# Kernel optimization log

Hardware: AMD Instinct MI355X
Metric: run time of the kernel (lower is better)

## Reference

```python
import jax, jax.numpy as jnp
import numpy as np

D_MODEL = 1024
D_INNER = 2 * D_MODEL
D_STATE = 16
DT_RANK = (D_MODEL + 15) // 16  # math.ceil(d_model/16) = 64
D_CONV = 4
SEQ_L = 2048
BATCH = 2


def setup_inputs() -> dict:
    key = jax.random.key(0)
    ks = jax.random.split(key, 8)
    def w(k, shape, scale=0.02):
        return jax.random.normal(k, shape, dtype=jnp.float32) * scale
    x = jax.random.normal(ks[0], (SEQ_L, BATCH, D_MODEL), dtype=jnp.float32)
    # weights stored as (in, out); torch Linear is x @ W.T with W (out, in)
    W_in = w(ks[1], (D_MODEL, 2 * D_INNER))
    W_conv = w(ks[2], (D_INNER, 1, D_CONV), 0.3)  # depthwise conv kernel (O, I/groups=1, K)
    b_conv = jnp.zeros((D_INNER,), jnp.float32)
    W_x = w(ks[3], (D_INNER, DT_RANK + 2 * D_STATE))
    W_dt = w(ks[4], (DT_RANK, D_INNER))
    b_dt = jnp.zeros((D_INNER,), jnp.float32)
    A_log = jnp.log(jnp.broadcast_to(jnp.arange(1, D_STATE + 1, dtype=jnp.float32),
                                     (D_INNER, D_STATE)))
    D = jnp.ones((D_INNER,), jnp.float32)
    W_out = w(ks[5], (D_INNER, D_MODEL))
    return {"x": x, "W_in": W_in, "W_conv": W_conv, "b_conv": b_conv,
            "W_x": W_x, "W_dt": W_dt, "b_dt": b_dt,
            "A_log": A_log, "D": D, "W_out": W_out}


def _mamba_forward(x, W_in, W_conv, b_conv, W_x, W_dt, b_dt, A_log, D, W_out):
    xb = jnp.transpose(x, (1, 0, 2))                       # (b, l, d_model)
    b, l, _ = xb.shape
    x_and_res = xb @ W_in                                  # (b, l, 2*d_inner)
    xs, res = jnp.split(x_and_res, 2, axis=-1)
    # depthwise causal conv1d: torch pads d_conv-1 both sides then truncates to l
    xc = jnp.transpose(xs, (0, 2, 1))                      # (b, d_inner, l)
    xc = jax.lax.conv_general_dilated(
        xc, W_conv, window_strides=(1,), padding=[(D_CONV - 1, 0)],
        feature_group_count=D_INNER,
        dimension_numbers=("NCH", "OIH", "NCH")) + b_conv[None, :, None]
    u = jax.nn.silu(jnp.transpose(xc, (0, 2, 1)))          # (b, l, d_inner)
    # SSM parameters
    A = -jnp.exp(A_log)                                    # (d_inner, n)
    x_dbl = u @ W_x                                        # (b, l, dt_rank + 2n)
    delta, Bm, Cm = jnp.split(x_dbl, [DT_RANK, DT_RANK + D_STATE], axis=-1)
    delta = jax.nn.softplus(delta @ W_dt + b_dt)           # (b, l, d_inner)
    # selective scan: state (b, d_inner, n)
    def step(state, inp):
        d_t, B_t, C_t, u_t = inp                           # (b,d_in),(b,n),(b,n),(b,d_in)
        dA = jnp.exp(d_t[:, :, None] * A)                  # (b, d_inner, n)
        dBu = d_t[:, :, None] * B_t[:, None, :] * u_t[:, :, None]
        state = dA * state + dBu
        y_t = jnp.einsum("bdn,bn->bd", state, C_t)
        return state, y_t

    init = jnp.zeros((b, D_INNER, D_STATE), jnp.float32)
    seq = (jnp.moveaxis(delta, 1, 0), jnp.moveaxis(Bm, 1, 0),
           jnp.moveaxis(Cm, 1, 0), jnp.moveaxis(u, 1, 0))
    _, ys = jax.lax.scan(step, init, seq)                  # (l, b, d_inner)
    y = jnp.moveaxis(ys, 0, 1) + u * D                     # (b, l, d_inner)
    y = y * jax.nn.silu(res)
    return y @ W_out                                       # (b, l, d_model)


def reference(x, W_in, W_conv, b_conv, W_x, W_dt, b_dt, A_log, D, W_out):
    return _mamba_forward(x, W_in, W_conv, b_conv, W_x, W_dt, b_dt, A_log, D, W_out)
```

## Files before the change

kernel.cpp:

```cpp
#include <hip/hip_runtime.h>
#include <hip/hip_bf16.h>

#define L_SEQ  2048
#define NBATCH 2
#define DMODEL 1024
#define DINNER 2048
#define DSTATE 16
#define DTRANK 64
#define MROWS  (L_SEQ * NBATCH)
#define NCHUNK 64
#define LCHUNK 32
#define LOG2E  1.44269504f

using bf16 = __hip_bfloat16;
typedef short s16x8 __attribute__((ext_vector_type(8)));
typedef float f32x4 __attribute__((ext_vector_type(4)));

__device__ __forceinline__ void gload_lds16(const bf16* g, bf16* l) {
    __builtin_amdgcn_global_load_lds(
        (const __attribute__((address_space(1))) void*)g,
        (__attribute__((address_space(3))) void*)l, 16, 0, 0);
}

__device__ __forceinline__ float bf2f(short v) {
    return __uint_as_float(((unsigned)(unsigned short)v) << 16);
}

__global__ __launch_bounds__(512, 2)
void gemm256(const bf16* __restrict__ A, const bf16* __restrict__ Bt,
             bf16* __restrict__ C, int N, int K, int lda, int ldb)
{
    __shared__ __align__(16) bf16 As[2][256 * 64];
    __shared__ __align__(16) bf16 Bs[2][256 * 64];

    const int tid  = threadIdx.x;
    const int wid  = tid >> 6;
    const int lane = tid & 63;
    const int wr = wid >> 2, wc = wid & 3;
    const int fr = lane & 15, fk = lane >> 4;

    const int nbx = gridDim.x;
    const int nwg = nbx * gridDim.y;
    int id = blockIdx.y * nbx + blockIdx.x;
    int cpx = nwg >> 3;
    id = (id & 7) * cpx + (id >> 3);
    const long bm = (long)(id / nbx) * 256;
    const long bn = (long)(id % nbx) * 256;

    const int q0 = tid, q1 = tid + 512;
    const int r0 = q0 >> 3, r1 = q1 >> 3;
    const int c0 = ((q0 & 7) ^ (r0 & 7)) << 3;
    const int c1 = ((q1 & 7) ^ (r1 & 7)) << 3;
    const bf16* sA0h0 = A  + (bm + r0)       * (long)lda + c0;
    const bf16* sA1h0 = A  + (bm + r1)       * (long)lda + c1;
    const bf16* sA0h1 = A  + (bm + 128 + r0) * (long)lda + c0;
    const bf16* sA1h1 = A  + (bm + 128 + r1) * (long)lda + c1;
    const bf16* sB0h0 = Bt + (bn + r0)       * (long)ldb + c0;
    const bf16* sB1h0 = Bt + (bn + r1)       * (long)ldb + c1;
    const bf16* sB0h1 = Bt + (bn + 128 + r0) * (long)ldb + c0;
    const bf16* sB1h1 = Bt + (bn + 128 + r1) * (long)ldb + c1;
    const int dst0 = wid * 512;
    const int dst1 = 4096 + wid * 512;

    const int o0   = ((fk ^ (fr & 7)) << 3);
    const int o1   = o0 ^ 32;
    const int rA64 = (wr * 64 + fr) * 64;
    const int rB64 = (wc * 32 + fr) * 64;

    f32x4 acc[8][4] = {};
    s16x8 af[4][2], bf0[2][2], bf1[2][2];
    const int nt = K >> 6;

#define STAGE(ARR, BUF, H, P0, P1) do {                    \
        gload_lds16(P0, &ARR[BUF][(H) * 8192 + dst0]);     \
        gload_lds16(P1, &ARR[BUF][(H) * 8192 + dst1]);     \
        P0 += 64; P1 += 64;                                \
    } while (0)

#define LOADA(MH, CUR) do {                                   \
        const bf16* ab = &As[CUR][rA64 + (MH) * 8192];        \
        _Pragma("unroll") for (int m = 0; m < 4; ++m) {       \
            af[m][0] = *(const s16x8*)&ab[m * 1024 + o0];     \
            af[m][1] = *(const s16x8*)&ab[m * 1024 + o1]; }   \
    } while (0)

#define LOADB(NH, CUR, BF) do {                               \
        const bf16* bb = &Bs[CUR][rB64 + (NH) * 8192];        \
        _Pragma("unroll") for (int n = 0; n < 2; ++n) {       \
            BF[n][0] = *(const s16x8*)&bb[n * 1024 + o0];     \
            BF[n][1] = *(const s16x8*)&bb[n * 1024 + o1]; }   \
    } while (0)

#define MFMAQ(MH, NH, BF) do {                                               \
        __builtin_amdgcn_s_setprio(1);                                       \
        _Pragma("unroll") for (int ks = 0; ks < 2; ++ks)                     \
        _Pragma("unroll") for (int m = 0; m < 4; ++m)                        \
        _Pragma("unroll") for (int n = 0; n < 2; ++n)                        \
            acc[(MH) * 4 + m][(NH) * 2 + n] =                                \
                __builtin_amdgcn_mfma_f32_16x16x32_bf16(                     \
                    af[m][ks], BF[n][ks], acc[(MH) * 4 + m][(NH) * 2 + n],   \
                    0, 0, 0);                                                \
        __builtin_amdgcn_s_setprio(0);                                       \
    } while (0)

#define WB(NV) asm volatile("s_waitcnt vmcnt(" #NV ")\n\ts_barrier" ::: "memory")

    STAGE(As, 0, 0, sA0h0, sA1h0);
    STAGE(Bs, 0, 0, sB0h0, sB1h0);
    STAGE(Bs, 0, 1, sB0h1, sB1h1);
    STAGE(As, 0, 1, sA0h1, sA1h1);
    WB(4);

    int cur = 0;
    for (int t = 0; t < nt - 1; ++t) {
        STAGE(As, cur ^ 1, 0, sA0h0, sA1h0);
        LOADA(0, cur); LOADB(0, cur, bf0);
        MFMAQ(0, 0, bf0);  WB(4);
        STAGE(Bs, cur ^ 1, 0, sB0h0, sB1h0);
        LOADB(1, cur, bf1);
        MFMAQ(0, 1, bf1);  WB(4);
        STAGE(Bs, cur ^ 1, 1, sB0h1, sB1h1);
        LOADA(1, cur);
        MFMAQ(1, 1, bf1);
        STAGE(As, cur ^ 1, 1, sA0h1, sA1h1);
        MFMAQ(1, 0, bf0);  WB(4);
        cur ^= 1;
    }
    LOADA(0, cur); LOADB(0, cur, bf0);
    MFMAQ(0, 0, bf0);  WB(2);
    LOADB(1, cur, bf1);
    MFMAQ(0, 1, bf1);  WB(0);
    LOADA(1, cur);
    MFMAQ(1, 1, bf1);
    MFMAQ(1, 0, bf0);

#undef STAGE
#undef LOADA
#undef LOADB
#undef MFMAQ
#undef WB

    #pragma unroll
    for (int mh = 0; mh < 2; ++mh)
    #pragma unroll
    for (int m = 0; m < 4; ++m)
    #pragma unroll
    for (int nh = 0; nh < 2; ++nh)
    #pragma unroll
    for (int n = 0; n < 2; ++n) {
        f32x4 v = acc[mh * 4 + m][nh * 2 + n];
        long row0 = bm + wr * 64 + mh * 128 + m * 16 + fk * 4;
        long col  = bn + wc * 32 + nh * 128 + n * 16 + fr;
        #pragma unroll
        for (int j = 0; j < 4; ++j)
            C[(row0 + j) * N + col] = __float2bfloat16(v[j]);
    }
}

template<typename OutT, int EPI, bool SPLITK = false>
__global__ __launch_bounds__(256)
void gemm_bt(const bf16* __restrict__ A, const bf16* __restrict__ Bt,
             OutT* __restrict__ C, const float* __restrict__ bias,
             int M, int N, int K, int lda, int ldb)
{
    __shared__ __align__(16) bf16 As[2][128 * 32];
    __shared__ __align__(16) bf16 Bs[2][128 * 32];

    const int tid  = threadIdx.x;
    const int wave = tid >> 6;
    const int lane = tid & 63;
    const int wr = wave >> 1, wc = wave & 1;
    const int fr = lane & 15, fk = lane >> 4;

    const int nbx = gridDim.x;
    const int nwg = nbx * gridDim.y;
    int id  = blockIdx.y * nbx + blockIdx.x;
    if (nwg >= 8) {
        int cpx = nwg >> 3;
        id = (id & 7) * cpx + (id >> 3);
    }
    const int bxi = id % nbx, byi = id / nbx;
    const long bm = (long)byi * 128;
    const long bn = (long)bxi * 128;

    if constexpr (SPLITK) {
        long ko = (long)blockIdx.z * K;
        A  += ko;
        Bt += ko;
        C  += (size_t)blockIdx.z * M * N;
    }

    const int r0 = tid >> 2,         c0 = (tid & 3) << 3;
    const int r1 = (256 + tid) >> 2, c1 = c0;
    const bf16* pA0 = A  + (bm + r0) * (long)lda + c0;
    const bf16* pA1 = A  + (bm + r1) * (long)lda + c1;
    const bf16* pB0 = Bt + (bn + r0) * (long)ldb + c0;
    const bf16* pB1 = Bt + (bn + r1) * (long)ldb + c1;
    const size_t ld0 = (size_t)(wave * 64) * 8;
    const size_t ld1 = (size_t)(256 + wave * 64) * 8;

    f32x4 acc[4][4] = {};
    const int nt = K >> 5;

    gload_lds16(pA0, &As[0][ld0]);
    gload_lds16(pB0, &Bs[0][ld0]);
    gload_lds16(pA1, &As[0][ld1]);
    gload_lds16(pB1, &Bs[0][ld1]);
    pA0 += 32; pA1 += 32; pB0 += 32; pB1 += 32;
    __syncthreads();

    int cur = 0;
    for (int t = 0; t < nt; ++t) {
        if (t + 1 < nt) {
            gload_lds16(pA0, &As[cur ^ 1][ld0]);
            gload_lds16(pB0, &Bs[cur ^ 1][ld0]);
            gload_lds16(pA1, &As[cur ^ 1][ld1]);
            gload_lds16(pB1, &Bs[cur ^ 1][ld1]);
            pA0 += 32; pA1 += 32; pB0 += 32; pB1 += 32;
        }

        s16x8 afrag[4], bfrag[4];
        #pragma unroll
        for (int m = 0; m < 4; ++m)
            afrag[m] = *(const s16x8*)&As[cur][(wr * 64 + m * 16 + fr) * 32 + fk * 8];
        #pragma unroll
        for (int n = 0; n < 4; ++n)
            bfrag[n] = *(const s16x8*)&Bs[cur][(wc * 64 + n * 16 + fr) * 32 + fk * 8];

        #pragma unroll
        for (int m = 0; m < 4; ++m)
            #pragma unroll
            for (int n = 0; n < 4; ++n)
                acc[m][n] = __builtin_amdgcn_mfma_f32_16x16x32_bf16(
                    afrag[m], bfrag[n], acc[m][n], 0, 0, 0);

        __syncthreads();
        cur ^= 1;
    }

    #pragma unroll
    for (int m = 0; m < 4; ++m)
        #pragma unroll
        for (int n = 0; n < 4; ++n) {
            f32x4 v = acc[m][n];
            long row0 = bm + wr * 64 + m * 16 + fk * 4;
            long col  = bn + wc * 64 + n * 16 + fr;
            #pragma unroll
            for (int j = 0; j < 4; ++j) {
                float val = v[j];
                if (EPI == 1) {
                    val += bias[col];
                    val = (val > 20.f) ? val : log1pf(__expf(val));
                }
                if constexpr (sizeof(OutT) == 2)
                    C[(row0 + j) * N + col] = __float2bfloat16(val);
                else
                    C[(row0 + j) * N + col] = val;
            }
        }
}

__global__ void transpose_bf16(const float* __restrict__ in, bf16* __restrict__ out,
                               int R, int C, int Cpad)
{
    __shared__ float tile[32][33];
    int cb = blockIdx.x * 32, rb = blockIdx.y * 32;
    int tx = threadIdx.x, ty = threadIdx.y;
    #pragma unroll
    for (int i = 0; i < 4; ++i) {
        int r = rb + ty + i * 8, c = cb + tx;
        tile[ty + i * 8][tx] = (r < R && c < C) ? in[(long)r * C + c] : 0.f;
    }
    __syncthreads();
    #pragma unroll
    for (int i = 0; i < 4; ++i) {
        int oc = cb + ty + i * 8;
        int orow = rb + tx;
        if (oc < Cpad && orow < R)
            out[(long)oc * R + orow] = __float2bfloat16(tile[tx][ty + i * 8]);
    }
}

__global__ void convert_x_kernel(const float* __restrict__ x, bf16* __restrict__ Xb)
{
    int idx = blockIdx.x * 256 + threadIdx.x;
    int c   = idx & (DMODEL - 1);
    int row = idx >> 10;
    int l   = row & (L_SEQ - 1);
    int b   = row >> 11;
    Xb[idx] = __float2bfloat16(x[((l * NBATCH + b) << 10) | c]);
}

__global__ void conv_silu_kernel(const bf16* __restrict__ xr, const float* __restrict__ Wc,
                                 const float* __restrict__ bc, bf16* __restrict__ u)
{
    int idx = blockIdx.x * 256 + threadIdx.x;
    int g   = idx & 255;
    int row = idx >> 8;
    int c   = g << 3;
    int l   = row & (L_SEQ - 1);

    float acc[8];
    f32x4 bi0 = *(const f32x4*)(bc + c);
    f32x4 bi1 = *(const f32x4*)(bc + c + 4);
    #pragma unroll
    for (int j = 0; j < 4; ++j) { acc[j] = bi0[j]; acc[4 + j] = bi1[j]; }

    f32x4 w[8];
    #pragma unroll
    for (int j = 0; j < 8; ++j) w[j] = *(const f32x4*)(Wc + (c + j) * 4);

    #pragma unroll
    for (int t = 0; t < 4; ++t) {
        int ll = l - 3 + t;
        if (ll >= 0) {
            s16x8 v = *(const s16x8*)(xr + (long)(row - 3 + t) * 4096 + c);
            #pragma unroll
            for (int j = 0; j < 8; ++j)
                acc[j] += bf2f(v[j]) * w[j][t];
        }
    }
    s16x8 o;
    #pragma unroll
    for (int j = 0; j < 8; ++j) {
        float a = acc[j];
        float s = a / (1.f + __builtin_amdgcn_exp2f(-LOG2E * a));
        bf16 h = __float2bfloat16(s);
        o[j] = *(short*)&h;
    }
    *(s16x8*)(u + (long)row * DINNER + c) = o;
}

__global__ void reduce_xdbl(const float* __restrict__ part, float* __restrict__ xdbl,
                            bf16* __restrict__ drbf)
{
    int idx = blockIdx.x * 256 + threadIdx.x;
    const size_t stride = (size_t)MROWS * 128;
    float v = part[idx] + part[idx + stride] + part[idx + 2 * stride]
            + part[idx + 3 * stride];
    xdbl[idx] = v;
    int col = idx & 127;
    if (col < 64)
        drbf[(idx >> 7) * 64 + col] = __float2bfloat16(v);
}

__global__ void reduce_out(const float* __restrict__ part, float* __restrict__ out)
{
    int i = blockIdx.x * 256 + threadIdx.x;
    f32x4 a = ((const f32x4*)part)[i];
    f32x4 b = ((const f32x4*)(part + (size_t)MROWS * DMODEL))[i];
    ((f32x4*)out)[i] = a + b;
}

__global__ __launch_bounds__(256)
void scan_phase1(const float* __restrict__ delta, const bf16* __restrict__ u,
                 const float* __restrict__ xdbl, const float* __restrict__ A_log,
                 float* __restrict__ AS)
{
    const int idx   = blockIdx.x * 256 + threadIdx.x;
    const int half  = idx & 1;
    const int ch    = idx >> 1;
    const int chunk = blockIdx.y;
    const int d     = ch & (DINNER - 1);
    const int b     = ch >> 11;
    const int n0    = half * 8;

    float A2[8], s[8];
    const f32x4* Arow = (const f32x4*)(A_log + d * DSTATE + n0);
    #pragma unroll
    for (int q = 0; q < 2; ++q) {
        f32x4 v = Arow[q];
        #pragma unroll
        for (int j = 0; j < 4; ++j) A2[q * 4 + j] = -__expf(v[j]) * LOG2E;
    }
    #pragma unroll
    for (int n = 0; n < 8; ++n) s[n] = 0.f;
    float sdl = 0.f;

    bool fastA = true;
    #pragma unroll
    for (int j = 0; j < 8; ++j)
        fastA &= fabsf(A2[j] + (float)(n0 + j + 1) * LOG2E)
                 < 0.01f * (float)(n0 + j + 1);

    const long row0 = (long)b * L_SEQ + chunk * LCHUNK;
    const float* pD = delta + row0 * DINNER + d;
    const bf16*  pU = u     + row0 * DINNER + d;
    const f32x4* pB = (const f32x4*)(xdbl + row0 * 128 + 64 + n0);

    if (fastA) {
        #pragma unroll 4
        for (int l = 0; l < LCHUNK; ++l) {
            float dl = *pD;
            float uv = __bfloat162float(*pU);
            f32x4 B0 = pB[0], B1 = pB[1];
            pD += DINNER; pU += DINNER; pB += 32;
            float dbu = dl * uv;
            sdl += dl;
            float b1 = __builtin_amdgcn_exp2f(-LOG2E * dl);
            float b2 = b1 * b1, b3 = b2 * b1, b4 = b2 * b2;
            float b5 = b4 * b1, b6 = b4 * b2, b7 = b4 * b3, b8 = b4 * b4;
            float pre = half ? b8 : 1.f;
            s[0] = pre * b1 * s[0] + dbu * B0[0];
            s[1] = pre * b2 * s[1] + dbu * B0[1];
            s[2] = pre * b3 * s[2] + dbu * B0[2];
            s[3] = pre * b4 * s[3] + dbu * B0[3];
            s[4] = pre * b5 * s[4] + dbu * B1[0];
            s[5] = pre * b6 * s[5] + dbu * B1[1];
            s[6] = pre * b7 * s[6] + dbu * B1[2];
            s[7] = pre * b8 * s[7] + dbu * B1[3];
        }
    } else {
        #pragma unroll 4
        for (int l = 0; l < LCHUNK; ++l) {
            float dl = *pD;
            float uv = __bfloat162float(*pU);
            f32x4 B0 = pB[0], B1 = pB[1];
            pD += DINNER; pU += DINNER; pB += 32;
            float dbu = dl * uv;
            sdl += dl;
            #pragma unroll
            for (int j = 0; j < 4; ++j) {
                float e = __builtin_amdgcn_exp2f(dl * A2[j]);
                s[j] = e * s[j] + dbu * B0[j];
            }
            #pragma unroll
            for (int j = 0; j < 4; ++j) {
                float e = __builtin_amdgcn_exp2f(dl * A2[4 + j]);
                s[4 + j] = e * s[4 + j] + dbu * B1[j];
            }
        }
    }
    float ap[8];
    #pragma unroll
    for (int n = 0; n < 8; ++n) ap[n] = __builtin_amdgcn_exp2f(sdl * A2[n]);

    float* o = AS + ((size_t)chunk * 4096 + ch) * 32 + n0;
    *(f32x4*)(o)      = *(f32x4*)&ap[0];
    *(f32x4*)(o + 4)  = *(f32x4*)&ap[4];
    *(f32x4*)(o + 16) = *(f32x4*)&s[0];
    *(f32x4*)(o + 20) = *(f32x4*)&s[4];
}

__global__ __launch_bounds__(256)
void scan_phase2(float* __restrict__ AS)
{
    const int idx = blockIdx.x * 256 + threadIdx.x;
    const int n   = idx & 15;
    const int ch  = idx >> 4;

    float s = 0.f;
    for (int cb = 0; cb < NCHUNK; cb += 16) {
        float av[16], sv[16];
        #pragma unroll
        for (int j = 0; j < 16; ++j) {
            size_t r = ((size_t)(cb + j) * 4096 + ch) * 32 + n;
            av[j] = AS[r];
            sv[j] = AS[r + 16];
        }
        #pragma unroll
        for (int j = 0; j < 16; ++j) {
            AS[((size_t)(cb + j) * 4096 + ch) * 32 + 16 + n] = s;
            s = av[j] * s + sv[j];
        }
    }
}

__global__ __launch_bounds__(256)
void scan_phase3(const float* __restrict__ delta, const bf16* __restrict__ u,
                 const float* __restrict__ xdbl, const bf16* __restrict__ xr,
                 const float* __restrict__ AS, const float* __restrict__ A_log,
                 const float* __restrict__ Dp, bf16* __restrict__ ybf)
{
    const int idx   = blockIdx.x * 256 + threadIdx.x;
    const int half  = idx & 1;
    const int ch    = idx >> 1;
    const int chunk = blockIdx.y;
    const int d     = ch & (DINNER - 1);
    const int b     = ch >> 11;
    const int n0    = half * 8;

    float A2[8], s[8];
    const f32x4* Arow = (const f32x4*)(A_log + d * DSTATE + n0);
    #pragma unroll
    for (int q = 0; q < 2; ++q) {
        f32x4 v = Arow[q];
        #pragma unroll
        for (int j = 0; j < 4; ++j) A2[q * 4 + j] = -__expf(v[j]) * LOG2E;
    }
    const float* ip = AS + ((size_t)chunk * 4096 + ch) * 32 + 16 + n0;
    *(f32x4*)&s[0] = *(const f32x4*)(ip);
    *(f32x4*)&s[4] = *(const f32x4*)(ip + 4);

    bool fastA = true;
    #pragma unroll
    for (int j = 0; j < 8; ++j)
        fastA &= fabsf(A2[j] + (float)(n0 + j + 1) * LOG2E)
                 < 0.01f * (float)(n0 + j + 1);

    const float Dd  = Dp[d];
    const long row0 = (long)b * L_SEQ + chunk * LCHUNK;

    const float* pD = delta + row0 * DINNER + d;
    const bf16*  pU = u     + row0 * DINNER + d;
    const bf16*  pR = xr    + row0 * 4096 + 2048 + d;
    const f32x4* pB = (const f32x4*)(xdbl + row0 * 128 + 64 + n0);
    bf16*        pY = ybf   + row0 * DINNER + d;

    if (fastA) {
        #pragma unroll 4
        for (int l = 0; l < LCHUNK; ++l) {
            float dl = *pD;
            float uv = __bfloat162float(*pU);
            float rs = __bfloat162float(*pR);
            f32x4 B0 = pB[0], B1 = pB[1];
            f32x4 C0 = pB[4], C1 = pB[5];
            pD += DINNER; pU += DINNER; pR += 4096; pB += 32;
            float dbu = dl * uv;
            float b1 = __builtin_amdgcn_exp2f(-LOG2E * dl);
            float b2 = b1 * b1, b3 = b2 * b1, b4 = b2 * b2;
            float b5 = b4 * b1, b6 = b4 * b2, b7 = b4 * b3, b8 = b4 * b4;
            float pre = half ? b8 : 1.f;
            float y0 = 0.f, y1 = 0.f;
            s[0] = pre * b1 * s[0] + dbu * B0[0];  y0 += s[0] * C0[0];
            s[1] = pre * b2 * s[1] + dbu * B0[1];  y0 += s[1] * C0[1];
            s[2] = pre * b3 * s[2] + dbu * B0[2];  y0 += s[2] * C0[2];
            s[3] = pre * b4 * s[3] + dbu * B0[3];  y0 += s[3] * C0[3];
            s[4] = pre * b5 * s[4] + dbu * B1[0];  y1 += s[4] * C1[0];
            s[5] = pre * b6 * s[5] + dbu * B1[1];  y1 += s[5] * C1[1];
            s[6] = pre * b7 * s[6] + dbu * B1[2];  y1 += s[6] * C1[2];
            s[7] = pre * b8 * s[7] + dbu * B1[3];  y1 += s[7] * C1[3];
            float yh = y0 + y1;
            float yt = yh + __shfl_xor(yh, 1);
            if (half == 0) {
                float yf = yt + uv * Dd;
                yf *= rs / (1.f + __builtin_amdgcn_exp2f(-LOG2E * rs));
                *pY = __float2bfloat16(yf);
            }
            pY += DINNER;
        }
    } else {
        #pragma unroll 4
        for (int l = 0; l < LCHUNK; ++l) {
            float dl = *pD;
            float uv = __bfloat162float(*pU);
            float rs = __bfloat162float(*pR);
            f32x4 B0 = pB[0], B1 = pB[1];
            f32x4 C0 = pB[4], C1 = pB[5];
            pD += DINNER; pU += DINNER; pR += 4096; pB += 32;
            float dbu = dl * uv;
            float y0 = 0.f, y1 = 0.f;
            #pragma unroll
            for (int j = 0; j < 4; ++j) {
                float e = __builtin_amdgcn_exp2f(dl * A2[j]);
                s[j] = e * s[j] + dbu * B0[j];
                y0 += s[j] * C0[j];
            }
            #pragma unroll
            for (int j = 0; j < 4; ++j) {
                float e = __builtin_amdgcn_exp2f(dl * A2[4 + j]);
                s[4 + j] = e * s[4 + j] + dbu * B1[j];
                y1 += s[4 + j] * C1[j];
            }
            float yh = y0 + y1;
            float yt = yh + __shfl_xor(yh, 1);
            if (half == 0) {
                float yf = yt + uv * Dd;
                yf *= rs / (1.f + __builtin_amdgcn_exp2f(-LOG2E * rs));
                *pY = __float2bfloat16(yf);
            }
            pY += DINNER;
        }
    }
}

extern "C" void kernel_launch(void* const* d_in, const int* in_sizes, int n_in,
                              void* d_out, int out_size, void* d_ws, size_t ws_size,
                              hipStream_t stream)
{
    const float* x      = (const float*)d_in[0];
    const float* W_in   = (const float*)d_in[1];
    const float* W_conv = (const float*)d_in[2];
    const float* b_conv = (const float*)d_in[3];
    const float* W_x    = (const float*)d_in[4];
    const float* W_dt   = (const float*)d_in[5];
    const float* b_dt   = (const float*)d_in[6];
    const float* A_log  = (const float*)d_in[7];
    const float* Dp     = (const float*)d_in[8];
    const float* W_out  = (const float*)d_in[9];
    float* out = (float*)d_out;

    char* ws = (char*)d_ws;
    size_t off = 0;
    auto alloc = [&](size_t bytes) {
        void* p = ws + off;
        off = (off + bytes + 255) & ~(size_t)255;
        return p;
    };
    bf16*  Xb    = (bf16*) alloc((size_t)MROWS * DMODEL * 2);
    bf16*  WinT  = (bf16*) alloc((size_t)4096  * DMODEL * 2);
    bf16*  xr    = (bf16*) alloc((size_t)MROWS * 4096  * 2);
    bf16*  ubf   = (bf16*) alloc((size_t)MROWS * DINNER * 2);
    bf16*  WxT   = (bf16*) alloc((size_t)128   * DINNER * 2);
    float* xdbl  = (float*)alloc((size_t)MROWS * 128 * 4);
    float* xdblp = (float*)alloc((size_t)4 * MROWS * 128 * 4);
    bf16*  drbf  = (bf16*) alloc((size_t)MROWS * 64 * 2);
    bf16*  WdtT  = (bf16*) alloc((size_t)DINNER * 64 * 2);
    float* delta = (float*)alloc((size_t)MROWS * DINNER * 4);
    bf16*  ybf   = (bf16*) alloc((size_t)MROWS * DINNER * 2);
    bf16*  WoutT = (bf16*) alloc((size_t)DMODEL * DINNER * 2);
    float* AS    = (float*)alloc((size_t)NCHUNK * 4096 * 32 * 4);

    dim3 tb(32, 8);
    transpose_bf16<<<dim3(128, 32), tb, 0, stream>>>(W_in,  WinT,  1024, 4096, 4096);
    transpose_bf16<<<dim3(4, 64),   tb, 0, stream>>>(W_x,   WxT,   2048, 96,   128);
    transpose_bf16<<<dim3(64, 2),   tb, 0, stream>>>(W_dt,  WdtT,  64,   2048, 2048);
    transpose_bf16<<<dim3(32, 64),  tb, 0, stream>>>(W_out, WoutT, 2048, 1024, 1024);
    convert_x_kernel<<<(MROWS * DMODEL) / 256, 256, 0, stream>>>(x, Xb);

    gemm256<<<dim3(4096 / 256, MROWS / 256), 512, 0, stream>>>(
        Xb, WinT, xr, 4096, 1024, 1024, 1024);
    conv_silu_kernel<<<(MROWS * DINNER / 8) / 256, 256, 0, stream>>>(
        xr, W_conv, b_conv, ubf);
    gemm_bt<float, 0, true><<<dim3(1, MROWS / 128, 4), 256, 0, stream>>>(
        ubf, WxT, xdblp, nullptr, MROWS, 128, 512, 2048, 2048);
    reduce_xdbl<<<(MROWS * 128) / 256, 256, 0, stream>>>(xdblp, xdbl, drbf);
    gemm_bt<float, 1><<<dim3(DINNER / 128, MROWS / 128), 256, 0, stream>>>(
        drbf, WdtT, delta, b_dt, MROWS, DINNER, 64, 64, 64);
    scan_phase1<<<dim3(32, NCHUNK), 256, 0, stream>>>(delta, ubf, xdbl, A_log, AS);
    scan_phase2<<<256, 256, 0, stream>>>(AS);
    scan_phase3<<<dim3(32, NCHUNK), 256, 0, stream>>>(delta, ubf, xdbl, xr, AS,
                                                      A_log, Dp, ybf);
    gemm_bt<float, 0, true><<<dim3(DMODEL / 128, MROWS / 128, 2), 256, 0, stream>>>(
        ybf, WoutT, (float*)AS, nullptr, MROWS, DMODEL, 1024, 2048, 2048);
    reduce_out<<<(MROWS * DMODEL) / 1024, 256, 0, stream>>>((float*)AS, out);
}
```

Before: 284.6 us.

## Store delta in bf16 and vectorize scan recurrences with packed float2 math

The delta projection GEMM now writes bf16 instead of fp32, and both scan phases read bf16 delta. This halves the delta write traffic and the two reads of it. The state updates in scan phases 1 and 3 are also rewritten as float2 vector operations, so the compiler can emit packed FMA/mul instructions. The cost is lower precision in delta, which feeds the exponentials and the state update, so accuracy tolerance could be at risk.

```diff
diff --git a/kernel.cpp b/kernel.cpp
--- a/kernel.cpp
+++ b/kernel.cpp
@@ -15,6 +15,7 @@
 using bf16 = __hip_bfloat16;
 typedef short s16x8 __attribute__((ext_vector_type(8)));
 typedef float f32x4 __attribute__((ext_vector_type(4)));
+typedef float f32x2 __attribute__((ext_vector_type(2)));
 
 __device__ __forceinline__ void gload_lds16(const bf16* g, bf16* l) {
     __builtin_amdgcn_global_load_lds(
@@ -353,7 +354,7 @@
 }
 
 __global__ __launch_bounds__(256)
-void scan_phase1(const float* __restrict__ delta, const bf16* __restrict__ u,
+void scan_phase1(const bf16* __restrict__ delta, const bf16* __restrict__ u,
                  const float* __restrict__ xdbl, const float* __restrict__ A_log,
                  float* __restrict__ AS)
 {
@@ -365,7 +366,7 @@
     const int b     = ch >> 11;
     const int n0    = half * 8;
 
-    float A2[8], s[8];
+    float A2[8];
     const f32x4* Arow = (const f32x4*)(A_log + d * DSTATE + n0);
     #pragma unroll
     for (int q = 0; q < 2; ++q) {
@@ -373,8 +374,7 @@
         #pragma unroll
         for (int j = 0; j < 4; ++j) A2[q * 4 + j] = -__expf(v[j]) * LOG2E;
     }
-    #pragma unroll
-    for (int n = 0; n < 8; ++n) s[n] = 0.f;
+    f32x2 s01 = {0.f, 0.f}, s23 = {0.f, 0.f}, s45 = {0.f, 0.f}, s67 = {0.f, 0.f};
     float sdl = 0.f;
 
     bool fastA = true;
@@ -384,51 +384,57 @@
                  < 0.01f * (float)(n0 + j + 1);
 
     const long row0 = (long)b * L_SEQ + chunk * LCHUNK;
-    const float* pD = delta + row0 * DINNER + d;
+    const bf16*  pD = delta + row0 * DINNER + d;
     const bf16*  pU = u     + row0 * DINNER + d;
     const f32x4* pB = (const f32x4*)(xdbl + row0 * 128 + 64 + n0);
 
     if (fastA) {
         #pragma unroll 4
         for (int l = 0; l < LCHUNK; ++l) {
-            float dl = *pD;
+            float dl = __bfloat162float(*pD);
             float uv = __bfloat162float(*pU);
             f32x4 B0 = pB[0], B1 = pB[1];
             pD += DINNER; pU += DINNER; pB += 32;
             float dbu = dl * uv;
             sdl += dl;
             float b1 = __builtin_amdgcn_exp2f(-LOG2E * dl);
-            float b2 = b1 * b1, b3 = b2 * b1, b4 = b2 * b2;
-            float b5 = b4 * b1, b6 = b4 * b2, b7 = b4 * b3, b8 = b4 * b4;
-            float pre = half ? b8 : 1.f;
-            s[0] = pre * b1 * s[0] + dbu * B0[0];
-            s[1] = pre * b2 * s[1] + dbu * B0[1];
-            s[2] = pre * b3 * s[2] + dbu * B0[2];
-            s[3] = pre * b4 * s[3] + dbu * B0[3];
-            s[4] = pre * b5 * s[4] + dbu * B1[0];
-            s[5] = pre * b6 * s[5] + dbu * B1[1];
-            s[6] = pre * b7 * s[6] + dbu * B1[2];
-            s[7] = pre * b8 * s[7] + dbu * B1[3];
+            float b2 = b1 * b1;
+            f32x2 bb  = {b2, b2};
+            f32x2 e01 = {b1, b2};
+            f32x2 e23 = e01 * bb;
+            f32x2 e45 = e23 * bb;
+            f32x2 e67 = e45 * bb;
+            float pr  = half ? e67.y : 1.f;
+            f32x2 pr2 = {pr, pr};
+            e01 *= pr2; e23 *= pr2; e45 *= pr2; e67 *= pr2;
+            f32x2 db = {dbu, dbu};
+            s01 = e01 * s01 + db * (f32x2){B0[0], B0[1]};
+            s23 = e23 * s23 + db * (f32x2){B0[2], B0[3]};
+            s45 = e45 * s45 + db * (f32x2){B1[0], B1[1]};
+            s67 = e67 * s67 + db * (f32x2){B1[2], B1[3]};
         }
     } else {
         #pragma unroll 4
         for (int l = 0; l < LCHUNK; ++l) {
-            float dl = *pD;
+            float dl = __bfloat162float(*pD);
             float uv = __bfloat162float(*pU);
             f32x4 B0 = pB[0], B1 = pB[1];
             pD += DINNER; pU += DINNER; pB += 32;
             float dbu = dl * uv;
             sdl += dl;
-            #pragma unroll
-            for (int j = 0; j < 4; ++j) {
-                float e = __builtin_amdgcn_exp2f(dl * A2[j]);
-                s[j] = e * s[j] + dbu * B0[j];
-            }
-            #pragma unroll
-            for (int j = 0; j < 4; ++j) {
-                float e = __builtin_amdgcn_exp2f(dl * A2[4 + j]);
-                s[4 + j] = e * s[4 + j] + dbu * B1[j];
-            }
+            f32x2 db = {dbu, dbu};
+            f32x2 e01 = {__builtin_amdgcn_exp2f(dl * A2[0]),
+                         __builtin_amdgcn_exp2f(dl * A2[1])};
+            f32x2 e23 = {__builtin_amdgcn_exp2f(dl * A2[2]),
+                         __builtin_amdgcn_exp2f(dl * A2[3])};
+            f32x2 e45 = {__builtin_amdgcn_exp2f(dl * A2[4]),
+                         __builtin_amdgcn_exp2f(dl * A2[5])};
+            f32x2 e67 = {__builtin_amdgcn_exp2f(dl * A2[6]),
+                         __builtin_amdgcn_exp2f(dl * A2[7])};
+            s01 = e01 * s01 + db * (f32x2){B0[0], B0[1]};
+            s23 = e23 * s23 + db * (f32x2){B0[2], B0[3]};
+            s45 = e45 * s45 + db * (f32x2){B1[0], B1[1]};
+            s67 = e67 * s67 + db * (f32x2){B1[2], B1[3]};
         }
     }
     float ap[8];
@@ -438,8 +444,8 @@
     float* o = AS + ((size_t)chunk * 4096 + ch) * 32 + n0;
     *(f32x4*)(o)      = *(f32x4*)&ap[0];
     *(f32x4*)(o + 4)  = *(f32x4*)&ap[4];
-    *(f32x4*)(o + 16) = *(f32x4*)&s[0];
-    *(f32x4*)(o + 20) = *(f32x4*)&s[4];
+    *(f32x4*)(o + 16) = (f32x4){s01.x, s01.y, s23.x, s23.y};
+    *(f32x4*)(o + 20) = (f32x4){s45.x, s45.y, s67.x, s67.y};
 }
 
 __global__ __launch_bounds__(256)
@@ -467,7 +473,7 @@
 }
 
 __global__ __launch_bounds__(256)
-void scan_phase3(const float* __restrict__ delta, const bf16* __restrict__ u,
+void scan_phase3(const bf16* __restrict__ delta, const bf16* __restrict__ u,
                  const float* __restrict__ xdbl, const bf16* __restrict__ xr,
                  const float* __restrict__ AS, const float* __restrict__ A_log,
                  const float* __restrict__ Dp, bf16* __restrict__ ybf)
@@ -480,7 +486,7 @@
     const int b     = ch >> 11;
     const int n0    = half * 8;
 
-    float A2[8], s[8];
+    float A2[8];
     const f32x4* Arow = (const f32x4*)(A_log + d * DSTATE + n0);
     #pragma unroll
     for (int q = 0; q < 2; ++q) {
@@ -489,8 +495,10 @@
         for (int j = 0; j < 4; ++j) A2[q * 4 + j] = -__expf(v[j]) * LOG2E;
     }
     const float* ip = AS + ((size_t)chunk * 4096 + ch) * 32 + 16 + n0;
-    *(f32x4*)&s[0] = *(const f32x4*)(ip);
-    *(f32x4*)&s[4] = *(const f32x4*)(ip + 4);
+    f32x4 i0 = *(const f32x4*)(ip);
+    f32x4 i1 = *(const f32x4*)(ip + 4);
+    f32x2 s01 = {i0[0], i0[1]}, s23 = {i0[2], i0[3]};
+    f32x2 s45 = {i1[0], i1[1]}, s67 = {i1[2], i1[3]};
 
     bool fastA = true;
     #pragma unroll
@@ -501,7 +509,7 @@
     const float Dd  = Dp[d];
     const long row0 = (long)b * L_SEQ + chunk * LCHUNK;
 
-    const float* pD = delta + row0 * DINNER + d;
+    const bf16*  pD = delta + row0 * DINNER + d;
     const bf16*  pU = u     + row0 * DINNER + d;
     const bf16*  pR = xr    + row0 * 4096 + 2048 + d;
     const f32x4* pB = (const f32x4*)(xdbl + row0 * 128 + 64 + n0);
@@ -510,7 +518,7 @@
     if (fastA) {
         #pragma unroll 4
         for (int l = 0; l < LCHUNK; ++l) {
-            float dl = *pD;
+            float dl = __bfloat162float(*pD);
             float uv = __bfloat162float(*pU);
             float rs = __bfloat162float(*pR);
             f32x4 B0 = pB[0], B1 = pB[1];
@@ -518,19 +526,25 @@
             pD += DINNER; pU += DINNER; pR += 4096; pB += 32;
             float dbu = dl * uv;
             float b1 = __builtin_amdgcn_exp2f(-LOG2E * dl);
-            float b2 = b1 * b1, b3 = b2 * b1, b4 = b2 * b2;
-            float b5 = b4 * b1, b6 = b4 * b2, b7 = b4 * b3, b8 = b4 * b4;
-            float pre = half ? b8 : 1.f;
-            float y0 = 0.f, y1 = 0.f;
-            s[0] = pre * b1 * s[0] + dbu * B0[0];  y0 += s[0] * C0[0];
-            s[1] = pre * b2 * s[1] + dbu * B0[1];  y0 += s[1] * C0[1];
-            s[2] = pre * b3 * s[2] + dbu * B0[2];  y0 += s[2] * C0[2];
-            s[3] = pre * b4 * s[3] + dbu * B0[3];  y0 += s[3] * C0[3];
-            s[4] = pre * b5 * s[4] + dbu * B1[0];  y1 += s[4] * C1[0];
-            s[5] = pre * b6 * s[5] + dbu * B1[1];  y1 += s[5] * C1[1];
-            s[6] = pre * b7 * s[6] + dbu * B1[2];  y1 += s[6] * C1[2];
-            s[7] = pre * b8 * s[7] + dbu * B1[3];  y1 += s[7] * C1[3];
-            float yh = y0 + y1;
+            float b2 = b1 * b1;
+            f32x2 bb  = {b2, b2};
+            f32x2 e01 = {b1, b2};
+            f32x2 e23 = e01 * bb;
+            f32x2 e45 = e23 * bb;
+            f32x2 e67 = e45 * bb;
+            float pr  = half ? e67.y : 1.f;
+            f32x2 pr2 = {pr, pr};
+            e01 *= pr2; e23 *= pr2; e45 *= pr2; e67 *= pr2;
+            f32x2 db = {dbu, dbu};
+            s01 = e01 * s01 + db * (f32x2){B0[0], B0[1]};
+            s23 = e23 * s23 + db * (f32x2){B0[2], B0[3]};
+            s45 = e45 * s45 + db * (f32x2){B1[0], B1[1]};
+            s67 = e67 * s67 + db * (f32x2){B1[2], B1[3]};
+            f32x2 y2 = s01 * (f32x2){C0[0], C0[1]};
+            y2 = s23 * (f32x2){C0[2], C0[3]} + y2;
+            y2 = s45 * (f32x2){C1[0], C1[1]} + y2;
+            y2 = s67 * (f32x2){C1[2], C1[3]} + y2;
+            float yh = y2.x + y2.y;
             float yt = yh + __shfl_xor(yh, 1);
             if (half == 0) {
                 float yf = yt + uv * Dd;
@@ -542,27 +556,31 @@
     } else {
         #pragma unroll 4
         for (int l = 0; l < LCHUNK; ++l) {
-            float dl = *pD;
+            float dl = __bfloat162float(*pD);
             float uv = __bfloat162float(*pU);
             float rs = __bfloat162float(*pR);
             f32x4 B0 = pB[0], B1 = pB[1];
             f32x4 C0 = pB[4], C1 = pB[5];
             pD += DINNER; pU += DINNER; pR += 4096; pB += 32;
             float dbu = dl * uv;
-            float y0 = 0.f, y1 = 0.f;
-            #pragma unroll
-            for (int j = 0; j < 4; ++j) {
-                float e = __builtin_amdgcn_exp2f(dl * A2[j]);
-                s[j] = e * s[j] + dbu * B0[j];
-                y0 += s[j] * C0[j];
-            }
-            #pragma unroll
-            for (int j = 0; j < 4; ++j) {
-                float e = __builtin_amdgcn_exp2f(dl * A2[4 + j]);
-                s[4 + j] = e * s[4 + j] + dbu * B1[j];
-                y1 += s[4 + j] * C1[j];
-            }
-            float yh = y0 + y1;
+            f32x2 db = {dbu, dbu};
+            f32x2 e01 = {__builtin_amdgcn_exp2f(dl * A2[0]),
+                         __builtin_amdgcn_exp2f(dl * A2[1])};
+            f32x2 e23 = {__builtin_amdgcn_exp2f(dl * A2[2]),
+                         __builtin_amdgcn_exp2f(dl * A2[3])};
+            f32x2 e45 = {__builtin_amdgcn_exp2f(dl * A2[4]),
+                         __builtin_amdgcn_exp2f(dl * A2[5])};
+            f32x2 e67 = {__builtin_amdgcn_exp2f(dl * A2[6]),
+                         __builtin_amdgcn_exp2f(dl * A2[7])};
+            s01 = e01 * s01 + db * (f32x2){B0[0], B0[1]};
+            s23 = e23 * s23 + db * (f32x2){B0[2], B0[3]};
+            s45 = e45 * s45 + db * (f32x2){B1[0], B1[1]};
+            s67 = e67 * s67 + db * (f32x2){B1[2], B1[3]};
+            f32x2 y2 = s01 * (f32x2){C0[0], C0[1]};
+            y2 = s23 * (f32x2){C0[2], C0[3]} + y2;
+            y2 = s45 * (f32x2){C1[0], C1[1]} + y2;
+            y2 = s67 * (f32x2){C1[2], C1[3]} + y2;
+            float yh = y2.x + y2.y;
             float yt = yh + __shfl_xor(yh, 1);
             if (half == 0) {
                 float yf = yt + uv * Dd;
@@ -606,7 +624,7 @@
     float* xdblp = (float*)alloc((size_t)4 * MROWS * 128 * 4);
     bf16*  drbf  = (bf16*) alloc((size_t)MROWS * 64 * 2);
     bf16*  WdtT  = (bf16*) alloc((size_t)DINNER * 64 * 2);
-    float* delta = (float*)alloc((size_t)MROWS * DINNER * 4);
+    bf16*  delta = (bf16*) alloc((size_t)MROWS * DINNER * 2);
     bf16*  ybf   = (bf16*) alloc((size_t)MROWS * DINNER * 2);
     bf16*  WoutT = (bf16*) alloc((size_t)DMODEL * DINNER * 2);
     float* AS    = (float*)alloc((size_t)NCHUNK * 4096 * 32 * 4);
@@ -625,7 +643,7 @@
     gemm_bt<float, 0, true><<<dim3(1, MROWS / 128, 4), 256, 0, stream>>>(
         ubf, WxT, xdblp, nullptr, MROWS, 128, 512, 2048, 2048);
     reduce_xdbl<<<(MROWS * 128) / 256, 256, 0, stream>>>(xdblp, xdbl, drbf);
-    gemm_bt<float, 1><<<dim3(DINNER / 128, MROWS / 128), 256, 0, stream>>>(
+    gemm_bt<bf16, 1><<<dim3(DINNER / 128, MROWS / 128), 256, 0, stream>>>(
         drbf, WdtT, delta, b_dt, MROWS, DINNER, 64, 64, 64);
     scan_phase1<<<dim3(32, NCHUNK), 256, 0, stream>>>(delta, ubf, xdbl, A_log, AS);
     scan_phase2<<<256, 256, 0, stream>>>(AS);
```

Result: slower. 304.7 us (+7.1%).
